# Kernel tuning notes

Hardware: AMD Instinct MI355X
Metric: run time of the kernel (lower is better)

## Reference

```python
import jax, jax.numpy as jnp
import numpy as np

N_NODES = 20000   # number of graph nodes
DEG = 16          # fixed out-degree -> ego-subgraph size n = DEG+1
N_T = 16          # N_templates
M_T = 8           # N_templates_nodes
D = 64            # N_features
ALPHA = 0.5       # FGW feature/structure trade-off
EPS = 0.1         # entropic regularization
N_OUTER = 4       # outer FGW (cost-relinearization) iterations
N_INNER = 10      # Sinkhorn iterations per outer step


def setup_inputs() -> dict:
    key = jax.random.key(0)
    k1, k2, k3, k4 = jax.random.split(key, 4)
    x = jax.random.normal(k1, (N_NODES, D), jnp.float32)
    # regular-degree edge list: node i owns edges [i*DEG, (i+1)*DEG)
    src = jnp.repeat(jnp.arange(N_NODES), DEG)
    dst = jax.random.randint(k2, (N_NODES * DEG,), 0, N_NODES)
    edge_index = jnp.stack([src, dst], axis=0)
    # templates_features: normal init, L2-normalized along feature dim (as in __init__)
    tf = jax.random.normal(k3, (N_T, M_T, D), jnp.float32)
    tf = tf / jnp.linalg.norm(tf, axis=2, keepdims=True)
    # template structure: normal init, L2-normalized dim 2, symmetrized (as in __init__)
    tm = jax.random.normal(k4, (N_T, M_T, M_T), jnp.float32)
    tm = tm / jnp.linalg.norm(tm, axis=2, keepdims=True)
    tm = 0.5 * (tm + jnp.swapaxes(tm, 1, 2))
    return {"x": x, "edge_index": edge_index, "templates_features": tf, "template": tm}


def _sinkhorn_log(cost, logp, logq):
    """Log-domain Sinkhorn. cost: [N,T,n,m]; returns transport plan [N,T,n,m]."""
    def step(carry, _):
        f, g = carry
        f = EPS * (logp - jax.nn.logsumexp((g[..., None, :] - cost) / EPS, axis=-1))
        g = EPS * (logq - jax.nn.logsumexp((f[..., :, None] - cost) / EPS, axis=-2))
        return (f, g), None
    f0 = jnp.zeros(cost.shape[:-1], cost.dtype)
    g0 = jnp.zeros(cost.shape[:-2] + (cost.shape[-1],), cost.dtype)
    (f, g), _ = jax.lax.scan(jax.checkpoint(step), (f0, g0), None, length=N_INNER)
    return jnp.exp((f[..., :, None] + g[..., None, :] - cost) / EPS)


def reference(x, edge_index, templates_features, template):
    N, d = x.shape
    neigh = edge_index[1].reshape(N, -1)                      # [N, K] neighbors per node
    K = neigh.shape[1]
    n = K + 1
    T, m, _ = templates_features.shape
    idx = jnp.concatenate([jnp.arange(N)[:, None], neigh], axis=1)  # [N, n] ego-subgraph nodes
    Floc = x[idx]                                             # [N, n, d] gathered features

    # feature cost M[N,T,n,m] = squared euclidean distance
    sqF = jnp.sum(Floc * Floc, axis=-1)                       # [N, n]
    sqT = jnp.sum(templates_features * templates_features, axis=-1)  # [T, m]
    Mcost = (sqF[:, None, :, None] + sqT[None, :, None, :]
             - 2.0 * jnp.einsum('Nnd,Tmd->NTnm', Floc, templates_features))

    # star ego-graph structure (center node connected to each neighbor), shared across nodes
    C1 = jnp.zeros((n, n), x.dtype).at[0, 1:].set(1.0).at[1:, 0].set(1.0)
    C2 = template                                             # [T, m, m] symmetric
    p = jnp.full((n,), 1.0 / n, x.dtype)
    q = jnp.full((m,), 1.0 / m, x.dtype)
    logp, logq = jnp.log(p), jnp.log(q)

    # constant part of GW tensor product (square loss): [1, T, n, m]
    a = (C1 * C1) @ p                                         # [n]
    b = jnp.einsum('Tmk,k->Tm', C2 * C2, q)                   # [T, m]
    constC = a[None, None, :, None] + b[None, :, None, :]

    def tens(G):
        # L(C1,C2) (x) G = constC - 2 * C1 G C2  (C2 symmetric)
        return constC - 2.0 * jnp.einsum('ij,NTjm,Tmk->NTik', C1, G, C2)

    G = jnp.broadcast_to((p[:, None] * q[None, :])[None, None], (N, T, n, m))
    for _ in range(N_OUTER):
        cost = (1.0 - ALPHA) * Mcost + ALPHA * tens(G)
        G = _sinkhorn_log(cost, logp, logq)

    # FGW value per (node, template): [N, T]
    fgw = jnp.sum(G * ((1.0 - ALPHA) * Mcost + ALPHA * tens(G)), axis=(-2, -1))
    return fgw
```

## Files before the change

### kernel.cpp

```cpp
#include <hip/hip_runtime.h>

#define DEG 16
#define TT 16
#define MM 8
#define MM2 4
#define NNR 8

#define C_SCALE 14.426950408889634f
#define PP (1.0f / 17.0f)
#define QVP 2.125f

#define TF_STRIDE 129
#define C2_STRIDE 65

typedef float f32x2 __attribute__((ext_vector_type(2)));

__global__ __launch_bounds__(256) void precomp(const float* __restrict__ x,
                                               const float* __restrict__ tf,
                                               float* __restrict__ P,
                                               float* __restrict__ sqn) {
  __shared__ float4 tf_lds[TT * TF_STRIDE];
  const float4* tf4g = (const float4*)tf;
  for (int i = threadIdx.x; i < TT * MM * 16; i += 256) {
    int tt = i >> 7, rem = i & 127;
    tf_lds[tt * TF_STRIDE + rem] = tf4g[i];
  }
  __syncthreads();

  int gid = blockIdx.x * 256 + (int)threadIdx.x;
  int i = gid >> 4, c = gid & 15;
  const float4* x4 = (const float4*)x + (size_t)i * 16;
  const float4* tfl = &tf_lds[c * TF_STRIDE];

  float acc[MM];
  float sq = 0.f;
#pragma unroll
  for (int m = 0; m < MM; ++m) acc[m] = 0.f;
  for (int k = 0; k < 16; ++k) {
    float4 xl = x4[k];
    sq += xl.x * xl.x + xl.y * xl.y + xl.z * xl.z + xl.w * xl.w;
#pragma unroll
    for (int m = 0; m < MM; ++m) {
      float4 tv = tfl[m * 16 + k];
      acc[m] += xl.x * tv.x + xl.y * tv.y + xl.z * tv.z + xl.w * tv.w;
    }
  }
  float4* Pr = (float4*)(P + (size_t)i * 128 + c * 8);
  Pr[0] = make_float4(acc[0], acc[1], acc[2], acc[3]);
  Pr[1] = make_float4(acc[4], acc[5], acc[6], acc[7]);
  if (c == 0) sqn[i] = sq;
}

__global__ __launch_bounds__(256)
void ltfgw_main(const float* __restrict__ P,
                const float* __restrict__ sqn,
                const int* __restrict__ dstRow,
                const float* __restrict__ c2g,
                float* __restrict__ out) {
  __shared__ float c2_lds[TT * C2_STRIDE];
  for (int i = threadIdx.x; i < TT * MM * MM; i += 256) {
    int tt = i >> 6, rem = i & 63;
    c2_lds[tt * C2_STRIDE + rem] = c2g[i];
  }
  __syncthreads();

  const int gid = blockIdx.x * 256 + (int)threadIdx.x;
  const int t = gid & 15;
  const int h = (gid >> 4) & 1;
  const int node = gid >> 5;
  const float hmask = (h == 0) ? 1.f : 0.f;
  const float* c2l = &c2_lds[t * C2_STRIDE];

  const float4* Pb = (const float4*)P;
  const int* nb = dstRow + node * DEG + h * NNR;

  f32x2 E2[NNR][MM2];
#pragma unroll
  for (int k = 0; k < NNR; ++k) {
    int idx = nb[k];
    float4 p0 = Pb[(size_t)idx * 32 + t * 2];
    float4 p1 = Pb[(size_t)idx * 32 + t * 2 + 1];
    float pv[MM] = {p0.x, p0.y, p0.z, p0.w, p1.x, p1.y, p1.z, p1.w};
    float pm = pv[0];
#pragma unroll
    for (int j = 1; j < MM; ++j) pm = fmaxf(pm, pv[j]);
#pragma unroll
    for (int j2 = 0; j2 < MM2; ++j2) {
      f32x2 e = {__builtin_amdgcn_exp2f(C_SCALE * (pv[2 * j2] - pm)),
                 __builtin_amdgcn_exp2f(C_SCALE * (pv[2 * j2 + 1] - pm))};
      E2[k][j2] = e;
    }
  }
  f32x2 e0c2[MM2];
  {
    float4 p0 = Pb[(size_t)node * 32 + t * 2];
    float4 p1 = Pb[(size_t)node * 32 + t * 2 + 1];
    float pv[MM] = {p0.x, p0.y, p0.z, p0.w, p1.x, p1.y, p1.z, p1.w};
    float pm = pv[0];
#pragma unroll
    for (int j = 1; j < MM; ++j) pm = fmaxf(pm, pv[j]);
#pragma unroll
    for (int j2 = 0; j2 < MM2; ++j2) {
      f32x2 e = {hmask * __builtin_amdgcn_exp2f(C_SCALE * (pv[2 * j2] - pm)),
                 hmask * __builtin_amdgcn_exp2f(C_SCALE * (pv[2 * j2 + 1] - pm))};
      e0c2[j2] = e;
    }
  }

#pragma unroll
  for (int j2 = 0; j2 < MM2; ++j2) {
    float t0v[2], t1v[2];
#pragma unroll
    for (int half = 0; half < 2; ++half) {
      int j = 2 * j2 + half;
      float s = 0.f, cs = 0.f;
#pragma unroll
      for (int k = 0; k < MM; ++k) {
        float a = c2l[j * MM + k];
        s += a * a;
        cs += c2l[k * MM + j];
      }
      float bq = 0.125f * s;
      t0v[half] = 0.5f * (16.f / 17.f + bq) - 0.125f * cs + cs * (1.f / 136.f);
      t1v[half] = 0.5f * (1.f / 17.f + bq) - cs * (1.f / 136.f);
    }
    f32x2 f0 = {__builtin_amdgcn_exp2f(-C_SCALE * t0v[0]),
                __builtin_amdgcn_exp2f(-C_SCALE * t0v[1])};
    f32x2 f1 = {__builtin_amdgcn_exp2f(-C_SCALE * t1v[0]),
                __builtin_amdgcn_exp2f(-C_SCALE * t1v[1])};
    e0c2[j2] *= f0;
#pragma unroll
    for (int k = 0; k < NNR; ++k) E2[k][j2] *= f1;
  }

  float g0_[MM];
#pragma unroll
  for (int j = 0; j < MM; ++j) g0_[j] = 1.f / 136.f;

  f32x2 v2[MM2];
  float u0, ureg[NNR];

  for (int outer = 0; outer < 4; ++outer) {
#pragma unroll
    for (int j2 = 0; j2 < MM2; ++j2) { f32x2 one = {1.f, 1.f}; v2[j2] = one; }
    for (int it = 0; it < 10; ++it) {
      f32x2 a0 = {(float)h, 0.f};
#pragma unroll
      for (int j2 = 0; j2 < MM2; ++j2) a0 += e0c2[j2] * v2[j2];
      u0 = __builtin_amdgcn_rcpf(a0.x + a0.y);
#pragma unroll
      for (int k = 0; k < NNR; ++k) {
        f32x2 a = E2[k][0] * v2[0];
#pragma unroll
        for (int j2 = 1; j2 < MM2; ++j2) a += E2[k][j2] * v2[j2];
        ureg[k] = __builtin_amdgcn_rcpf(a.x + a.y);
      }
      f32x2 part2[MM2];
#pragma unroll
      for (int j2 = 0; j2 < MM2; ++j2) part2[j2] = e0c2[j2] * u0;
#pragma unroll
      for (int k = 0; k < NNR; ++k) {
        float uk = ureg[k];
#pragma unroll
        for (int j2 = 0; j2 < MM2; ++j2) part2[j2] += E2[k][j2] * uk;
      }
#pragma unroll
      for (int j2 = 0; j2 < MM2; ++j2) {
        part2[j2].x += __shfl_xor(part2[j2].x, 16);
        part2[j2].y += __shfl_xor(part2[j2].y, 16);
      }
#pragma unroll
      for (int j2 = 0; j2 < MM2; ++j2) {
        f32x2 r = {__builtin_amdgcn_rcpf(part2[j2].x),
                   __builtin_amdgcn_rcpf(part2[j2].y)};
        v2[j2] = QVP * r;
      }
    }
    float g0n[MM];
#pragma unroll
    for (int j2 = 0; j2 < MM2; ++j2) {
      f32x2 e0u = e0c2[j2] * u0;
      e0u.x += __shfl_xor(e0u.x, 16);
      e0u.y += __shfl_xor(e0u.y, 16);
      g0n[2 * j2]     = PP * v2[j2].x * e0u.x;
      g0n[2 * j2 + 1] = PP * v2[j2].y * e0u.y;
    }
    if (outer < 3) {
      float dg[MM];
#pragma unroll
      for (int j = 0; j < MM; ++j) dg[j] = g0n[j] - g0_[j];
#pragma unroll
      for (int j2 = 0; j2 < MM2; ++j2) {
        float av[2];
#pragma unroll
        for (int half = 0; half < 2; ++half) {
          int j = 2 * j2 + half;
          float d = 0.f;
#pragma unroll
          for (int k = 0; k < MM; ++k) d += dg[k] * c2l[k * MM + j];
          av[half] = C_SCALE * d;
        }
        f32x2 cfp = {__builtin_amdgcn_exp2f(av[0]), __builtin_amdgcn_exp2f(av[1])};
        f32x2 cfm = {__builtin_amdgcn_exp2f(-av[0]), __builtin_amdgcn_exp2f(-av[1])};
        e0c2[j2] *= cfm;
#pragma unroll
        for (int k = 0; k < NNR; ++k) E2[k][j2] *= cfp;
      }
    }
#pragma unroll
    for (int j = 0; j < MM; ++j) g0_[j] = g0n[j];
  }

  float T0p[MM];
  float tens1 = 0.f;
#pragma unroll
  for (int j = 0; j < MM; ++j) {
    float s = 0.f, cs = 0.f, gd = 0.f;
#pragma unroll
    for (int k = 0; k < MM; ++k) {
      float a = c2l[j * MM + k];
      s += a * a;
      cs += c2l[k * MM + j];
      gd += g0_[k] * c2l[k * MM + j];
    }
    float bq = 0.125f * s;
    T0p[j] = 0.5f * (16.f / 17.f + bq) - 0.125f * cs + gd;
    float T1p = 0.5f * (1.f / 17.f + bq) - gd;
    tens1 += (0.125f - g0_[j]) * T1p;
  }
  float fgr = 0.f;
#pragma unroll
  for (int k = 0; k < NNR; ++k) {
    int idx = nb[k];
    float4 p0 = Pb[(size_t)idx * 32 + t * 2];
    float4 p1 = Pb[(size_t)idx * 32 + t * 2 + 1];
    float pv[MM] = {p0.x, p0.y, p0.z, p0.w, p1.x, p1.y, p1.z, p1.w};
    float hh = 0.5f * (sqn[idx] + 1.0f);
    f32x2 acc = {0.f, 0.f};
#pragma unroll
    for (int j2 = 0; j2 < MM2; ++j2) {
      f32x2 mh = {hh - pv[2 * j2], hh - pv[2 * j2 + 1]};
      acc += (E2[k][j2] * v2[j2]) * mh;
    }
    fgr += ureg[k] * (acc.x + acc.y);
  }
  float fg = PP * fgr;
  {
    float4 p0 = Pb[(size_t)node * 32 + t * 2];
    float4 p1 = Pb[(size_t)node * 32 + t * 2 + 1];
    float pv[MM] = {p0.x, p0.y, p0.z, p0.w, p1.x, p1.y, p1.z, p1.w};
    float hh0 = 0.5f * (sqn[node] + 1.0f);
    float r0 = 0.f;
#pragma unroll
    for (int j = 0; j < MM; ++j) r0 += g0_[j] * (hh0 - pv[j] + T0p[j]);
    fg += hmask * (r0 + tens1);
  }
  fg += __shfl_xor(fg, 16);
  if (h == 0) out[node * TT + t] = fg;
}

extern "C" void kernel_launch(void* const* d_in, const int* in_sizes, int n_in,
                              void* d_out, int out_size, void* d_ws, size_t ws_size,
                              hipStream_t stream) {
  const float* x  = (const float*)d_in[0];
  const int*   ei = (const int*)d_in[1];
  const float* tf = (const float*)d_in[2];
  const float* c2 = (const float*)d_in[3];
  const int* dstRow = ei + (in_sizes[1] / 2);
  int n_nodes = in_sizes[0] / 64;

  float* P   = (float*)d_ws;
  float* sqn = P + (size_t)n_nodes * 128;
  float* out = (float*)d_out;

  int threadsA = n_nodes * 16;
  precomp<<<(threadsA + 255) / 256, 256, 0, stream>>>(x, tf, P, sqn);
  int lanesB = out_size * 2;
  ltfgw_main<<<(lanesB + 255) / 256, 256, 0, stream>>>(P, sqn, dstRow, c2, out);
}
```

Baseline: 215.8 us.

## Pack FP32 math into vec2 ops, fold Sinkhorn scale constants, two nodes per precomp thread

The precompute kernel now has each thread handle two nodes, with templates re-laid out in LDS so packed two-wide FMAs can be used. The main kernel folds the q and p scaling factors into a constant shift (QSH) applied to the exponentials, which removes the per-iteration multiply by QVP. It also rebalances the Sinkhorn sums into vec2 trees and fuses the v update with the cross-lane shuffle. The previous-iteration g0 values move to LDS to reduce register pressure. The risks are changed numerics from the rescaling and extra LDS traffic for g0.

```diff
diff --git a/kernel.cpp b/kernel.cpp
--- a/kernel.cpp
+++ b/kernel.cpp
@@ -7,48 +7,69 @@
 #define NNR 8
 
 #define C_SCALE 14.426950408889634f
-#define PP (1.0f / 17.0f)
-#define QVP 2.125f
-
-#define TF_STRIDE 129
-#define C2_STRIDE 65
+#define QSH 0.07537716f
+#define GS 0.125f
+
+#define TFP_PITCH 516
+#define C2_STRIDE 66
+#define G0_STRIDE 9
 
 typedef float f32x2 __attribute__((ext_vector_type(2)));
+
+static __device__ __forceinline__ f32x2 mk2(float a, float b) { f32x2 r; r.x = a; r.y = b; return r; }
+static __device__ __forceinline__ f32x2 exp2_pk(f32x2 a) {
+  return mk2(__builtin_amdgcn_exp2f(a.x), __builtin_amdgcn_exp2f(a.y));
+}
 
 __global__ __launch_bounds__(256) void precomp(const float* __restrict__ x,
                                                const float* __restrict__ tf,
                                                float* __restrict__ P,
                                                float* __restrict__ sqn) {
-  __shared__ float4 tf_lds[TT * TF_STRIDE];
+  __shared__ float tf_i[TT * TFP_PITCH];
   const float4* tf4g = (const float4*)tf;
   for (int i = threadIdx.x; i < TT * MM * 16; i += 256) {
-    int tt = i >> 7, rem = i & 127;
-    tf_lds[tt * TF_STRIDE + rem] = tf4g[i];
+    int r = i >> 4, ck = i & 15;
+    int tt = r >> 3, m = r & 7, m2 = m >> 1, half = m & 1;
+    float4 v = tf4g[i];
+    float* base = &tf_i[tt * TFP_PITCH + m2 * 128 + ck * 8 + half];
+    base[0] = v.x; base[2] = v.y; base[4] = v.z; base[6] = v.w;
   }
   __syncthreads();
 
   int gid = blockIdx.x * 256 + (int)threadIdx.x;
-  int i = gid >> 4, c = gid & 15;
-  const float4* x4 = (const float4*)x + (size_t)i * 16;
-  const float4* tfl = &tf_lds[c * TF_STRIDE];
-
-  float acc[MM];
-  float sq = 0.f;
-#pragma unroll
-  for (int m = 0; m < MM; ++m) acc[m] = 0.f;
+  int pairI = gid >> 4, c = gid & 15;
+  int n0 = pairI * 2, n1 = n0 + 1;
+  const float4* xa4 = (const float4*)x + (size_t)n0 * 16;
+  const float4* xb4 = (const float4*)x + (size_t)n1 * 16;
+  const float* tfl = &tf_i[c * TFP_PITCH];
+
+  f32x2 accA[MM2], accB[MM2], sq2A = mk2(0.f, 0.f), sq2B = mk2(0.f, 0.f);
+#pragma unroll
+  for (int m2 = 0; m2 < MM2; ++m2) { accA[m2] = mk2(0.f, 0.f); accB[m2] = mk2(0.f, 0.f); }
+
   for (int k = 0; k < 16; ++k) {
-    float4 xl = x4[k];
-    sq += xl.x * xl.x + xl.y * xl.y + xl.z * xl.z + xl.w * xl.w;
-#pragma unroll
-    for (int m = 0; m < MM; ++m) {
-      float4 tv = tfl[m * 16 + k];
-      acc[m] += xl.x * tv.x + xl.y * tv.y + xl.z * tv.z + xl.w * tv.w;
-    }
-  }
-  float4* Pr = (float4*)(P + (size_t)i * 128 + c * 8);
-  Pr[0] = make_float4(acc[0], acc[1], acc[2], acc[3]);
-  Pr[1] = make_float4(acc[4], acc[5], acc[6], acc[7]);
-  if (c == 0) sqn[i] = sq;
+    float4 xa = xa4[k], xb = xb4[k];
+    sq2A += mk2(xa.x, xa.y) * mk2(xa.x, xa.y) + mk2(xa.z, xa.w) * mk2(xa.z, xa.w);
+    sq2B += mk2(xb.x, xb.y) * mk2(xb.x, xb.y) + mk2(xb.z, xb.w) * mk2(xb.z, xb.w);
+#pragma unroll
+    for (int m2 = 0; m2 < MM2; ++m2) {
+      const float4* tq = (const float4*)(tfl + m2 * 128 + k * 8);
+      float4 q0 = tq[0], q1 = tq[1];
+      accA[m2] += (mk2(q0.x, q0.y) * xa.x + mk2(q0.z, q0.w) * xa.y)
+                + (mk2(q1.x, q1.y) * xa.z + mk2(q1.z, q1.w) * xa.w);
+      accB[m2] += (mk2(q0.x, q0.y) * xb.x + mk2(q0.z, q0.w) * xb.y)
+                + (mk2(q1.x, q1.y) * xb.z + mk2(q1.z, q1.w) * xb.w);
+    }
+  }
+#pragma unroll
+  for (int m2 = 0; m2 < MM2; ++m2) {
+    *(f32x2*)(P + (size_t)n0 * 128 + c * 8 + 2 * m2) = accA[m2];
+    *(f32x2*)(P + (size_t)n1 * 128 + c * 8 + 2 * m2) = accB[m2];
+  }
+  if (c == 0) {
+    sqn[n0] = sq2A.x + sq2A.y;
+    sqn[n1] = sq2B.x + sq2B.y;
+  }
 }
 
 __global__ __launch_bounds__(256)
@@ -58,18 +79,21 @@
                 const float* __restrict__ c2g,
                 float* __restrict__ out) {
   __shared__ float c2_lds[TT * C2_STRIDE];
+  __shared__ float g0_lds[128 * G0_STRIDE];
   for (int i = threadIdx.x; i < TT * MM * MM; i += 256) {
     int tt = i >> 6, rem = i & 63;
     c2_lds[tt * C2_STRIDE + rem] = c2g[i];
   }
   __syncthreads();
 
-  const int gid = blockIdx.x * 256 + (int)threadIdx.x;
+  const int tid = (int)threadIdx.x;
+  const int gid = blockIdx.x * 256 + tid;
   const int t = gid & 15;
   const int h = (gid >> 4) & 1;
   const int node = gid >> 5;
   const float hmask = (h == 0) ? 1.f : 0.f;
   const float* c2l = &c2_lds[t * C2_STRIDE];
+  float* g0p = &g0_lds[((int)((tid >> 5) << 4) | (tid & 15)) * G0_STRIDE];
 
   const float4* Pb = (const float4*)P;
   const int* nb = dstRow + node * DEG + h * NNR;
@@ -80,31 +104,25 @@
     int idx = nb[k];
     float4 p0 = Pb[(size_t)idx * 32 + t * 2];
     float4 p1 = Pb[(size_t)idx * 32 + t * 2 + 1];
-    float pv[MM] = {p0.x, p0.y, p0.z, p0.w, p1.x, p1.y, p1.z, p1.w};
-    float pm = pv[0];
-#pragma unroll
-    for (int j = 1; j < MM; ++j) pm = fmaxf(pm, pv[j]);
-#pragma unroll
-    for (int j2 = 0; j2 < MM2; ++j2) {
-      f32x2 e = {__builtin_amdgcn_exp2f(C_SCALE * (pv[2 * j2] - pm)),
-                 __builtin_amdgcn_exp2f(C_SCALE * (pv[2 * j2 + 1] - pm))};
-      E2[k][j2] = e;
-    }
+    float pm = fmaxf(fmaxf(fmaxf(p0.x, p0.y), fmaxf(p0.z, p0.w)),
+                     fmaxf(fmaxf(p1.x, p1.y), fmaxf(p1.z, p1.w)));
+    float pmc = -C_SCALE * pm;
+    E2[k][0] = exp2_pk(mk2(p0.x, p0.y) * C_SCALE + pmc);
+    E2[k][1] = exp2_pk(mk2(p0.z, p0.w) * C_SCALE + pmc);
+    E2[k][2] = exp2_pk(mk2(p1.x, p1.y) * C_SCALE + pmc);
+    E2[k][3] = exp2_pk(mk2(p1.z, p1.w) * C_SCALE + pmc);
   }
   f32x2 e0c2[MM2];
   {
     float4 p0 = Pb[(size_t)node * 32 + t * 2];
     float4 p1 = Pb[(size_t)node * 32 + t * 2 + 1];
-    float pv[MM] = {p0.x, p0.y, p0.z, p0.w, p1.x, p1.y, p1.z, p1.w};
-    float pm = pv[0];
-#pragma unroll
-    for (int j = 1; j < MM; ++j) pm = fmaxf(pm, pv[j]);
-#pragma unroll
-    for (int j2 = 0; j2 < MM2; ++j2) {
-      f32x2 e = {hmask * __builtin_amdgcn_exp2f(C_SCALE * (pv[2 * j2] - pm)),
-                 hmask * __builtin_amdgcn_exp2f(C_SCALE * (pv[2 * j2 + 1] - pm))};
-      e0c2[j2] = e;
-    }
+    float pm = fmaxf(fmaxf(fmaxf(p0.x, p0.y), fmaxf(p0.z, p0.w)),
+                     fmaxf(fmaxf(p1.x, p1.y), fmaxf(p1.z, p1.w)));
+    float pmc = -C_SCALE * pm;
+    e0c2[0] = hmask * exp2_pk(mk2(p0.x, p0.y) * C_SCALE + pmc);
+    e0c2[1] = hmask * exp2_pk(mk2(p0.z, p0.w) * C_SCALE + pmc);
+    e0c2[2] = hmask * exp2_pk(mk2(p1.x, p1.y) * C_SCALE + pmc);
+    e0c2[3] = hmask * exp2_pk(mk2(p1.z, p1.w) * C_SCALE + pmc);
   }
 
 #pragma unroll
@@ -121,94 +139,76 @@
         cs += c2l[k * MM + j];
       }
       float bq = 0.125f * s;
-      t0v[half] = 0.5f * (16.f / 17.f + bq) - 0.125f * cs + cs * (1.f / 136.f);
-      t1v[half] = 0.5f * (1.f / 17.f + bq) - cs * (1.f / 136.f);
-    }
-    f32x2 f0 = {__builtin_amdgcn_exp2f(-C_SCALE * t0v[0]),
-                __builtin_amdgcn_exp2f(-C_SCALE * t0v[1])};
-    f32x2 f1 = {__builtin_amdgcn_exp2f(-C_SCALE * t1v[0]),
-                __builtin_amdgcn_exp2f(-C_SCALE * t1v[1])};
-    e0c2[j2] *= f0;
+      t0v[half] = 0.5f * (16.f / 17.f + bq) - 0.125f * cs + cs * (1.f / 136.f) + QSH;
+      t1v[half] = 0.5f * (1.f / 17.f + bq) - cs * (1.f / 136.f) + QSH;
+    }
+    e0c2[j2] *= exp2_pk(mk2(-C_SCALE * t0v[0], -C_SCALE * t0v[1]));
+    f32x2 f1 = exp2_pk(mk2(-C_SCALE * t1v[0], -C_SCALE * t1v[1]));
 #pragma unroll
     for (int k = 0; k < NNR; ++k) E2[k][j2] *= f1;
   }
 
-  float g0_[MM];
-#pragma unroll
-  for (int j = 0; j < MM; ++j) g0_[j] = 1.f / 136.f;
-
+#pragma unroll
+  for (int j = 0; j < MM; ++j) g0p[j] = 1.f / 136.f;
+
+  float g0c[MM];
   f32x2 v2[MM2];
   float u0, ureg[NNR];
 
   for (int outer = 0; outer < 4; ++outer) {
 #pragma unroll
-    for (int j2 = 0; j2 < MM2; ++j2) { f32x2 one = {1.f, 1.f}; v2[j2] = one; }
+    for (int j2 = 0; j2 < MM2; ++j2) v2[j2] = mk2(1.f, 1.f);
     for (int it = 0; it < 10; ++it) {
-      f32x2 a0 = {(float)h, 0.f};
-#pragma unroll
-      for (int j2 = 0; j2 < MM2; ++j2) a0 += e0c2[j2] * v2[j2];
-      u0 = __builtin_amdgcn_rcpf(a0.x + a0.y);
+      f32x2 a01 = e0c2[0] * v2[0] + e0c2[1] * v2[1];
+      f32x2 a23 = e0c2[2] * v2[2] + e0c2[3] * v2[3];
+      f32x2 a = a01 + a23;
+      u0 = __builtin_amdgcn_rcpf((float)h + (a.x + a.y));
 #pragma unroll
       for (int k = 0; k < NNR; ++k) {
-        f32x2 a = E2[k][0] * v2[0];
-#pragma unroll
-        for (int j2 = 1; j2 < MM2; ++j2) a += E2[k][j2] * v2[j2];
-        ureg[k] = __builtin_amdgcn_rcpf(a.x + a.y);
-      }
-      f32x2 part2[MM2];
-#pragma unroll
-      for (int j2 = 0; j2 < MM2; ++j2) part2[j2] = e0c2[j2] * u0;
-#pragma unroll
-      for (int k = 0; k < NNR; ++k) {
-        float uk = ureg[k];
-#pragma unroll
-        for (int j2 = 0; j2 < MM2; ++j2) part2[j2] += E2[k][j2] * uk;
+        f32x2 b01 = E2[k][0] * v2[0] + E2[k][1] * v2[1];
+        f32x2 b23 = E2[k][2] * v2[2] + E2[k][3] * v2[3];
+        f32x2 b = b01 + b23;
+        ureg[k] = __builtin_amdgcn_rcpf(b.x + b.y);
       }
 #pragma unroll
       for (int j2 = 0; j2 < MM2; ++j2) {
-        part2[j2].x += __shfl_xor(part2[j2].x, 16);
-        part2[j2].y += __shfl_xor(part2[j2].y, 16);
-      }
-#pragma unroll
-      for (int j2 = 0; j2 < MM2; ++j2) {
-        f32x2 r = {__builtin_amdgcn_rcpf(part2[j2].x),
-                   __builtin_amdgcn_rcpf(part2[j2].y)};
-        v2[j2] = QVP * r;
-      }
-    }
-    float g0n[MM];
+        f32x2 s0 = e0c2[j2] * u0      + E2[0][j2] * ureg[0];
+        f32x2 s1 = E2[1][j2] * ureg[1] + E2[2][j2] * ureg[2];
+        f32x2 s2 = E2[3][j2] * ureg[3] + E2[4][j2] * ureg[4];
+        f32x2 s3 = E2[5][j2] * ureg[5] + E2[6][j2] * ureg[6];
+        f32x2 s4 = E2[7][j2] * ureg[7];
+        f32x2 part = ((s0 + s1) + (s2 + s3)) + s4;
+        part.x += __shfl_xor(part.x, 16);
+        part.y += __shfl_xor(part.y, 16);
+        v2[j2] = mk2(__builtin_amdgcn_rcpf(part.x), __builtin_amdgcn_rcpf(part.y));
+      }
+    }
 #pragma unroll
     for (int j2 = 0; j2 < MM2; ++j2) {
       f32x2 e0u = e0c2[j2] * u0;
       e0u.x += __shfl_xor(e0u.x, 16);
       e0u.y += __shfl_xor(e0u.y, 16);
-      g0n[2 * j2]     = PP * v2[j2].x * e0u.x;
-      g0n[2 * j2 + 1] = PP * v2[j2].y * e0u.y;
+      g0c[2 * j2]     = GS * v2[j2].x * e0u.x;
+      g0c[2 * j2 + 1] = GS * v2[j2].y * e0u.y;
     }
     if (outer < 3) {
       float dg[MM];
 #pragma unroll
-      for (int j = 0; j < MM; ++j) dg[j] = g0n[j] - g0_[j];
+      for (int j = 0; j < MM; ++j) { dg[j] = g0c[j] - g0p[j]; g0p[j] = g0c[j]; }
+      const f32x2* c2p = (const f32x2*)c2l;
 #pragma unroll
       for (int j2 = 0; j2 < MM2; ++j2) {
-        float av[2];
-#pragma unroll
-        for (int half = 0; half < 2; ++half) {
-          int j = 2 * j2 + half;
-          float d = 0.f;
-#pragma unroll
-          for (int k = 0; k < MM; ++k) d += dg[k] * c2l[k * MM + j];
-          av[half] = C_SCALE * d;
-        }
-        f32x2 cfp = {__builtin_amdgcn_exp2f(av[0]), __builtin_amdgcn_exp2f(av[1])};
-        f32x2 cfm = {__builtin_amdgcn_exp2f(-av[0]), __builtin_amdgcn_exp2f(-av[1])};
-        e0c2[j2] *= cfm;
+        f32x2 d01 = dg[0] * c2p[0 * MM2 + j2] + dg[1] * c2p[1 * MM2 + j2];
+        f32x2 d23 = dg[2] * c2p[2 * MM2 + j2] + dg[3] * c2p[3 * MM2 + j2];
+        f32x2 d45 = dg[4] * c2p[4 * MM2 + j2] + dg[5] * c2p[5 * MM2 + j2];
+        f32x2 d67 = dg[6] * c2p[6 * MM2 + j2] + dg[7] * c2p[7 * MM2 + j2];
+        f32x2 av = ((d01 + d23) + (d45 + d67)) * C_SCALE;
+        e0c2[j2] *= exp2_pk(mk2(-av.x, -av.y));
+        f32x2 cfp = exp2_pk(av);
 #pragma unroll
         for (int k = 0; k < NNR; ++k) E2[k][j2] *= cfp;
       }
     }
-#pragma unroll
-    for (int j = 0; j < MM; ++j) g0_[j] = g0n[j];
   }
 
   float T0p[MM];
@@ -221,12 +221,12 @@
       float a = c2l[j * MM + k];
       s += a * a;
       cs += c2l[k * MM + j];
-      gd += g0_[k] * c2l[k * MM + j];
+      gd += g0c[k] * c2l[k * MM + j];
     }
     float bq = 0.125f * s;
     T0p[j] = 0.5f * (16.f / 17.f + bq) - 0.125f * cs + gd;
     float T1p = 0.5f * (1.f / 17.f + bq) - gd;
-    tens1 += (0.125f - g0_[j]) * T1p;
+    tens1 += (0.125f - g0c[j]) * T1p;
   }
   float fgr = 0.f;
 #pragma unroll
@@ -234,17 +234,14 @@
     int idx = nb[k];
     float4 p0 = Pb[(size_t)idx * 32 + t * 2];
     float4 p1 = Pb[(size_t)idx * 32 + t * 2 + 1];
-    float pv[MM] = {p0.x, p0.y, p0.z, p0.w, p1.x, p1.y, p1.z, p1.w};
     float hh = 0.5f * (sqn[idx] + 1.0f);
-    f32x2 acc = {0.f, 0.f};
-#pragma unroll
-    for (int j2 = 0; j2 < MM2; ++j2) {
-      f32x2 mh = {hh - pv[2 * j2], hh - pv[2 * j2 + 1]};
-      acc += (E2[k][j2] * v2[j2]) * mh;
-    }
+    f32x2 acc = (E2[k][0] * v2[0]) * (hh - mk2(p0.x, p0.y))
+              + (E2[k][1] * v2[1]) * (hh - mk2(p0.z, p0.w))
+              + (E2[k][2] * v2[2]) * (hh - mk2(p1.x, p1.y))
+              + (E2[k][3] * v2[3]) * (hh - mk2(p1.z, p1.w));
     fgr += ureg[k] * (acc.x + acc.y);
   }
-  float fg = PP * fgr;
+  float fg = GS * fgr;
   {
     float4 p0 = Pb[(size_t)node * 32 + t * 2];
     float4 p1 = Pb[(size_t)node * 32 + t * 2 + 1];
@@ -252,7 +249,7 @@
     float hh0 = 0.5f * (sqn[node] + 1.0f);
     float r0 = 0.f;
 #pragma unroll
-    for (int j = 0; j < MM; ++j) r0 += g0_[j] * (hh0 - pv[j] + T0p[j]);
+    for (int j = 0; j < MM; ++j) r0 += g0c[j] * (hh0 - pv[j] + T0p[j]);
     fg += hmask * (r0 + tens1);
   }
   fg += __shfl_xor(fg, 16);
@@ -273,7 +270,7 @@
   float* sqn = P + (size_t)n_nodes * 128;
   float* out = (float*)d_out;
 
-  int threadsA = n_nodes * 16;
+  int threadsA = (n_nodes / 2) * 16;
   precomp<<<(threadsA + 255) / 256, 256, 0, stream>>>(x, tf, P, sqn);
   int lanesB = out_size * 2;
   ltfgw_main<<<(lanesB + 255) / 256, 256, 0, stream>>>(P, sqn, dstRow, c2, out);
```

After: 223.5 us. 3.6% more time.
